# Kernel optimization log

Hardware: AMD Instinct MI355X
Metric: run time of the kernel (lower is better)

Reference implementation:

```python
import jax, jax.numpy as jnp
from jax import lax
import numpy as np

H = 64  # hidden_dim


def _lstm_dir(x, W_ih, W_hh, b, reverse):
    # x: [B,T,I]; W_ih: [4H,I]; W_hh: [4H,H]; b: [4H] (b_ih+b_hh combined)
    B = x.shape[0]
    xp = jnp.einsum('bti,gi->btg', x, W_ih) + b          # [B,T,4H]
    xp = jnp.swapaxes(xp, 0, 1)                          # [T,B,4H]

    def step(carry, xt):
        h, c = carry
        g = xt + h @ W_hh.T                              # [B,4H]
        i, f, gg, o = jnp.split(g, 4, axis=-1)           # PyTorch gate order i,f,g,o
        i = jax.nn.sigmoid(i)
        f = jax.nn.sigmoid(f)
        gg = jnp.tanh(gg)
        o = jax.nn.sigmoid(o)
        c = f * c + i * gg
        h = o * jnp.tanh(c)
        return (h, c), h

    init = (jnp.zeros((B, H), x.dtype), jnp.zeros((B, H), x.dtype))
    _, hs = lax.scan(step, init, xp, reverse=reverse)    # outputs aligned to original positions
    return jnp.swapaxes(hs, 0, 1)                        # [B,T,H]


def _bilstm_layer(x, Wih_f, Whh_f, b_f, Wih_b, Whh_b, b_b):
    fwd = _lstm_dir(x, Wih_f, Whh_f, b_f, reverse=False)
    bwd = _lstm_dir(x, Wih_b, Whh_b, b_b, reverse=True)
    return jnp.concatenate([fwd, bwd], axis=-1)          # [B,T,2H]


def setup_inputs() -> dict:
    key = jax.random.key(0)
    ks = jax.random.split(key, 16)
    s = 0.1
    d = {}
    d['x'] = jax.random.normal(ks[0], (512, 512, 4), dtype=jnp.float32)
    # layer 0 (input size 4), forward / backward directions
    d['Wih_l0_f'] = jax.random.normal(ks[1], (4 * H, 4)) * s
    d['Whh_l0_f'] = jax.random.normal(ks[2], (4 * H, H)) * s
    d['b_l0_f'] = jax.random.normal(ks[3], (4 * H,)) * s
    d['Wih_l0_b'] = jax.random.normal(ks[4], (4 * H, 4)) * s
    d['Whh_l0_b'] = jax.random.normal(ks[5], (4 * H, H)) * s
    d['b_l0_b'] = jax.random.normal(ks[6], (4 * H,)) * s
    # layer 1 (input size 2H = 128)
    d['Wih_l1_f'] = jax.random.normal(ks[7], (4 * H, 2 * H)) * s
    d['Whh_l1_f'] = jax.random.normal(ks[8], (4 * H, H)) * s
    d['b_l1_f'] = jax.random.normal(ks[9], (4 * H,)) * s
    d['Wih_l1_b'] = jax.random.normal(ks[10], (4 * H, 2 * H)) * s
    d['Whh_l1_b'] = jax.random.normal(ks[11], (4 * H, H)) * s
    d['b_l1_b'] = jax.random.normal(ks[12], (4 * H,)) * s
    # final linear: 2H -> 1
    d['fc_w'] = jax.random.normal(ks[13], (1, 2 * H)) * s
    d['fc_b'] = jax.random.normal(ks[14], (1,)) * s
    return d


def reference(x, Wih_l0_f, Whh_l0_f, b_l0_f, Wih_l0_b, Whh_l0_b, b_l0_b,
              Wih_l1_f, Whh_l1_f, b_l1_f, Wih_l1_b, Whh_l1_b, b_l1_b,
              fc_w, fc_b):
    h0 = _bilstm_layer(x, Wih_l0_f, Whh_l0_f, b_l0_f, Wih_l0_b, Whh_l0_b, b_l0_b)
    h1 = _bilstm_layer(h0, Wih_l1_f, Whh_l1_f, b_l1_f, Wih_l1_b, Whh_l1_b, b_l1_b)
    pooled = jnp.mean(h1, axis=1)                        # [B,2H]
    return pooled @ fc_w.T + fc_b                        # [B,1]
```

## Files before the change

kernel.cpp:

```cpp
#include <hip/hip_runtime.h>

#define H  64
#define TT 512
#define BB 512
#define CSTR 80
#define UCH 16
#define XSTRF 260

typedef _Float16 half8 __attribute__((ext_vector_type(8)));
typedef float    f32x4 __attribute__((ext_vector_type(4)));

__device__ __forceinline__ float frcp(float x) { return __builtin_amdgcn_rcpf(x); }
__device__ __forceinline__ float sigm(float x) { return frcp(1.f + __expf(-x)); }
__device__ __forceinline__ float tanh_fast(float x) { return 1.f - 2.f * frcp(__expf(2.f * x) + 1.f); }

__global__ __launch_bounds__(256) void xpad_prep(const float* __restrict__ x,
                                                 _Float16* __restrict__ xpad) {
    int gid = blockIdx.x * 256 + threadIdx.x;
    int row = gid >> 2, q = gid & 3;
    half8 v = {0,0,0,0,0,0,0,0};
    if (q == 0) {
        float4 xv = ((const float4*)x)[row];
        v[0] = (_Float16)xv.x; v[1] = (_Float16)xv.y;
        v[2] = (_Float16)xv.z; v[3] = (_Float16)xv.w;
    }
    *(half8*)(xpad + (size_t)row * 32 + q * 8) = v;
}

__global__ __launch_bounds__(256, 2) void lstm_l0(
    const _Float16* __restrict__ xpad,
    const float* __restrict__ WihF, const float* __restrict__ WhhF, const float* __restrict__ bF,
    const float* __restrict__ WihB, const float* __restrict__ WhhB, const float* __restrict__ bB,
    _Float16* __restrict__ out0)
{
    const int dir = blockIdx.x & 1;
    const int b0  = (blockIdx.x >> 1) * 2;
    const int tid = threadIdx.x;
    const int w = tid >> 6, l = tid & 63, m = l & 15, q = l >> 4;
    const int ch  = m & 1;
    const int ubo = (m >> 1) & 3;
    const int uo  = w * 16 + ubo * 4 + q;
    const bool act = (m < 8);

    const float* Wih = dir ? WihB : WihF;
    const float* Whh = dir ? WhhB : WhhF;
    const float* bia = dir ? bB   : bF;

    half8 Ah[4][2];
#pragma unroll
    for (int ub = 0; ub < 4; ++ub) {
        const int wrow = (m & 3) * 64 + (w * 16 + ub * 4 + (m >> 2));
#pragma unroll
        for (int s2 = 0; s2 < 2; ++s2) {
            const float* src = Whh + wrow * 64 + s2 * 32 + q * 8;
            half8 tmp;
#pragma unroll
            for (int j = 0; j < 8; ++j) tmp[j] = (_Float16)src[j];
            Ah[ub][s2] = tmp;
        }
    }

    half8 Bg[4];
    float bvj[4];
#pragma unroll
    for (int j = 0; j < 4; ++j) {
        const int n  = w * 64 + j * 16 + m;
        const int gr = (n & 3) * 64 + (n >> 2);
        bvj[j] = bia[gr];
        half8 tmp;
#pragma unroll
        for (int jj = 0; jj < 8; ++jj) {
            int k = q * 8 + jj;
            tmp[jj] = (k < 4) ? (_Float16)Wih[gr * 4 + k] : (_Float16)0.f;
        }
        Bg[j] = tmp;
    }

    __shared__ __align__(16) float xp[2][UCH][XSTRF];
    __shared__ _Float16 hbuf[2][2][CSTR];
    for (int i = tid; i < 2 * 2 * CSTR / 2; i += 256) ((unsigned int*)hbuf)[i] = 0u;
    __syncthreads();

    float c = 0.f;
    int p = 0;

    for (int chunk = 0; chunk < TT / UCH; ++chunk) {
        const int c0 = chunk * UCH;

#pragma unroll
        for (int cc = 0; cc < 2; ++cc) {
            const int tA = dir ? (TT - 1 - (c0 + m)) : (c0 + m);
            half8 a0 = *(const half8*)(xpad + (size_t)((b0 + cc) * TT + tA) * 32 + q * 8);
#pragma unroll
            for (int j = 0; j < 4; ++j) {
                f32x4 acc = {bvj[j], bvj[j], bvj[j], bvj[j]};
                acc = __builtin_amdgcn_mfma_f32_16x16x32_f16(a0, Bg[j], acc, 0, 0, 0);
#pragma unroll
                for (int i = 0; i < 4; ++i)
                    xp[cc][q * 4 + i][w * 64 + j * 16 + m] = acc[i];
            }
        }

        f32x4 xv = *(const f32x4*)&xp[ch][0][uo * 4];
        for (int u = 0; u < UCH; ++u) {
            int un = (u + 1 < UCH) ? (u + 1) : u;
            f32x4 xn = *(const f32x4*)&xp[ch][un][uo * 4];

            half8 ah0 = *(const half8*)&hbuf[p][ch][q * 8];
            half8 ah1 = *(const half8*)&hbuf[p][ch][32 + q * 8];

            f32x4 g_own;
#pragma unroll
            for (int ub = 0; ub < 4; ++ub) {
                f32x4 a = __builtin_amdgcn_mfma_f32_16x16x32_f16(Ah[ub][0], ah0, xv, 0, 0, 0);
                a       = __builtin_amdgcn_mfma_f32_16x16x32_f16(Ah[ub][1], ah1, a, 0, 0, 0);
                if (ub == ubo) g_own = a;
            }

            float e_i = sigm(g_own[0]), e_f = sigm(g_own[1]);
            float e_g = tanh_fast(g_own[2]), e_o = sigm(g_own[3]);
            c = e_f * c + e_i * e_g;
            float hh = e_o * tanh_fast(c);

            if (act) {
                const int tg = dir ? (TT - 1 - (c0 + u)) : (c0 + u);
                out0[((size_t)(b0 + ch) * TT + tg) * 128 + dir * 64 + uo] = (_Float16)hh;
                hbuf[p ^ 1][ch][uo] = (_Float16)hh;
            }
            __syncthreads();
            p ^= 1; xv = xn;
        }
    }
}

__global__ __launch_bounds__(256, 2) void lstm_l1(
    const _Float16* __restrict__ out0,
    const float* __restrict__ WihF, const float* __restrict__ WhhF, const float* __restrict__ bF,
    const float* __restrict__ WihB, const float* __restrict__ WhhB, const float* __restrict__ bB,
    float* __restrict__ pooled)
{
    const int dir = blockIdx.x & 1;
    const int b0  = (blockIdx.x >> 1) * 2;
    const int tid = threadIdx.x;
    const int w = tid >> 6, l = tid & 63, m = l & 15, q = l >> 4;
    const int ch  = m & 1;
    const int ubo = (m >> 1) & 3;
    const int uo  = w * 16 + ubo * 4 + q;
    const bool act = (m < 8);

    const float* Wih = dir ? WihB : WihF;
    const float* Whh = dir ? WhhB : WhhF;
    const float* bia = dir ? bB   : bF;

    half8 Ah[4][2];
#pragma unroll
    for (int ub = 0; ub < 4; ++ub) {
        const int wrow = (m & 3) * 64 + (w * 16 + ub * 4 + (m >> 2));
#pragma unroll
        for (int s2 = 0; s2 < 2; ++s2) {
            const float* src = Whh + wrow * 64 + s2 * 32 + q * 8;
            half8 tmp;
#pragma unroll
            for (int j = 0; j < 8; ++j) tmp[j] = (_Float16)src[j];
            Ah[ub][s2] = tmp;
        }
    }

    half8 Bg[4][4];
    float bvj[4];
#pragma unroll
    for (int j = 0; j < 4; ++j) {
        const int n  = w * 64 + j * 16 + m;
        const int gr = (n & 3) * 64 + (n >> 2);
        bvj[j] = bia[gr];
#pragma unroll
        for (int k4 = 0; k4 < 4; ++k4) {
            const float* src = Wih + gr * 128 + k4 * 32 + q * 8;
            half8 tmp;
#pragma unroll
            for (int jj = 0; jj < 8; ++jj) tmp[jj] = (_Float16)src[jj];
            Bg[j][k4] = tmp;
        }
    }

    __shared__ __align__(16) float xp[2][UCH][XSTRF];
    __shared__ _Float16 hbuf[2][2][CSTR];
    for (int i = tid; i < 2 * 2 * CSTR / 2; i += 256) ((unsigned int*)hbuf)[i] = 0u;
    __syncthreads();

    float c = 0.f, hs = 0.f;
    int p = 0;

    for (int chunk = 0; chunk < TT / UCH; ++chunk) {
        const int c0 = chunk * UCH;

#pragma unroll
        for (int cc = 0; cc < 2; ++cc) {
            const int tA = dir ? (TT - 1 - (c0 + m)) : (c0 + m);
            const _Float16* arow = out0 + (size_t)((b0 + cc) * TT + tA) * 128 + q * 8;
            half8 a0 = *(const half8*)(arow);
            half8 a1 = *(const half8*)(arow + 32);
            half8 a2 = *(const half8*)(arow + 64);
            half8 a3 = *(const half8*)(arow + 96);
#pragma unroll
            for (int j = 0; j < 4; ++j) {
                f32x4 acc = {bvj[j], bvj[j], bvj[j], bvj[j]};
                acc = __builtin_amdgcn_mfma_f32_16x16x32_f16(a0, Bg[j][0], acc, 0, 0, 0);
                acc = __builtin_amdgcn_mfma_f32_16x16x32_f16(a1, Bg[j][1], acc, 0, 0, 0);
                acc = __builtin_amdgcn_mfma_f32_16x16x32_f16(a2, Bg[j][2], acc, 0, 0, 0);
                acc = __builtin_amdgcn_mfma_f32_16x16x32_f16(a3, Bg[j][3], acc, 0, 0, 0);
#pragma unroll
                for (int i = 0; i < 4; ++i)
                    xp[cc][q * 4 + i][w * 64 + j * 16 + m] = acc[i];
            }
        }

        f32x4 xv = *(const f32x4*)&xp[ch][0][uo * 4];
        for (int u = 0; u < UCH; ++u) {
            int un = (u + 1 < UCH) ? (u + 1) : u;
            f32x4 xn = *(const f32x4*)&xp[ch][un][uo * 4];

            half8 ah0 = *(const half8*)&hbuf[p][ch][q * 8];
            half8 ah1 = *(const half8*)&hbuf[p][ch][32 + q * 8];

            f32x4 g_own;
#pragma unroll
            for (int ub = 0; ub < 4; ++ub) {
                f32x4 a = __builtin_amdgcn_mfma_f32_16x16x32_f16(Ah[ub][0], ah0, xv, 0, 0, 0);
                a       = __builtin_amdgcn_mfma_f32_16x16x32_f16(Ah[ub][1], ah1, a, 0, 0, 0);
                if (ub == ubo) g_own = a;
            }

            float e_i = sigm(g_own[0]), e_f = sigm(g_own[1]);
            float e_g = tanh_fast(g_own[2]), e_o = sigm(g_own[3]);
            c = e_f * c + e_i * e_g;
            float hh = e_o * tanh_fast(c);
            hs += hh;

            if (act) hbuf[p ^ 1][ch][uo] = (_Float16)hh;
            __syncthreads();
            p ^= 1; xv = xn;
        }
    }

    if (act) pooled[(size_t)(b0 + ch) * 128 + dir * 64 + uo] = hs;
}

__global__ __launch_bounds__(64) void fc_head(
    const float* __restrict__ pooled,
    const float* __restrict__ fcw, const float* __restrict__ fcb,
    float* __restrict__ out)
{
    const int b = blockIdx.x;
    const int l = threadIdx.x;
    float v = pooled[b * 128 + l] * fcw[l] + pooled[b * 128 + 64 + l] * fcw[64 + l];
#pragma unroll
    for (int o = 32; o > 0; o >>= 1) v += __shfl_down(v, o);
    if (l == 0) out[b] = v * (1.f / (float)TT) + fcb[0];
}

extern "C" void kernel_launch(void* const* d_in, const int* in_sizes, int n_in,
                              void* d_out, int out_size, void* d_ws, size_t ws_size,
                              hipStream_t stream) {
    const float* x       = (const float*)d_in[0];
    const float* Wih_l0f = (const float*)d_in[1];
    const float* Whh_l0f = (const float*)d_in[2];
    const float* b_l0f   = (const float*)d_in[3];
    const float* Wih_l0b = (const float*)d_in[4];
    const float* Whh_l0b = (const float*)d_in[5];
    const float* b_l0b   = (const float*)d_in[6];
    const float* Wih_l1f = (const float*)d_in[7];
    const float* Whh_l1f = (const float*)d_in[8];
    const float* b_l1f   = (const float*)d_in[9];
    const float* Wih_l1b = (const float*)d_in[10];
    const float* Whh_l1b = (const float*)d_in[11];
    const float* b_l1b   = (const float*)d_in[12];
    const float* fcw     = (const float*)d_in[13];
    const float* fcb     = (const float*)d_in[14];

    const size_t o_xpad   = 0;
    const size_t o_out0   = o_xpad + (size_t)BB * TT * 32 * 2;
    const size_t o_pooled = o_out0 + (size_t)BB * TT * 128 * 2;

    _Float16* xpad   = (_Float16*)((char*)d_ws + o_xpad);
    _Float16* out0   = (_Float16*)((char*)d_ws + o_out0);
    float*    pooled = (float*)((char*)d_ws + o_pooled);

    xpad_prep<<<(BB * TT * 4) / 256, 256, 0, stream>>>(x, xpad);
    lstm_l0<<<(BB / 2) * 2, 256, 0, stream>>>(xpad, Wih_l0f, Whh_l0f, b_l0f,
                                              Wih_l0b, Whh_l0b, b_l0b, out0);
    lstm_l1<<<(BB / 2) * 2, 256, 0, stream>>>(out0, Wih_l1f, Whh_l1f, b_l1f,
                                              Wih_l1b, Whh_l1b, b_l1b, pooled);
    fc_head<<<BB, 64, 0, stream>>>(pooled, fcw, fcb, (float*)d_out);
}
```

Measured before the change: 482.7 us.

## Rewrite LSTM kernels: one wave per sequence, barrier-free recurrence, prescaled exp2 gates

Merges the two layer kernels into one template in which each wavefront owns a whole batch row and computes all 256 gates with 16 MFMA tiles, so the per-step block barrier disappears. Gate weights and biases are prescaled by log2e factors so activations use exp2 with combined reciprocals. Input projections for the next chunk are interleaved into the recurrent step, with global loads issued two chunks ahead. In exchange each wave does four times the recurrent MFMA work, occupancy drops to one block per SM with larger LDS and register use, and the grid halves to 256 blocks.

```diff
diff --git a/kernel.cpp b/kernel.cpp
--- a/kernel.cpp
+++ b/kernel.cpp
@@ -1,18 +1,22 @@
 #include <hip/hip_runtime.h>
 
-#define H  64
-#define TT 512
-#define BB 512
-#define CSTR 80
-#define UCH 16
-#define XSTRF 260
+#define H   64
+#define TT  512
+#define BB  512
+#define UCH 8
+#define NCH (TT / UCH)
+#define XSTR 260
 
 typedef _Float16 half8 __attribute__((ext_vector_type(8)));
 typedef float    f32x4 __attribute__((ext_vector_type(4)));
 
+#define LOG2E 1.4426950408889634f
+#define TWOL  2.8853900817779268f
+
+#define MFMA16 __builtin_amdgcn_mfma_f32_16x16x32_f16
+
 __device__ __forceinline__ float frcp(float x) { return __builtin_amdgcn_rcpf(x); }
-__device__ __forceinline__ float sigm(float x) { return frcp(1.f + __expf(-x)); }
-__device__ __forceinline__ float tanh_fast(float x) { return 1.f - 2.f * frcp(__expf(2.f * x) + 1.f); }
+__device__ __forceinline__ float ex2(float x)  { return __builtin_amdgcn_exp2f(x); }
 
 __global__ __launch_bounds__(256) void xpad_prep(const float* __restrict__ x,
                                                  _Float16* __restrict__ xpad) {
@@ -27,223 +31,170 @@
     *(half8*)(xpad + (size_t)row * 32 + q * 8) = v;
 }
 
-__global__ __launch_bounds__(256, 2) void lstm_l0(
-    const _Float16* __restrict__ xpad,
+
+template<int KS, bool IS_L0>
+__global__ __launch_bounds__(256, 1) void lstm_k(
+    const _Float16* __restrict__ xsrc,
     const float* __restrict__ WihF, const float* __restrict__ WhhF, const float* __restrict__ bF,
     const float* __restrict__ WihB, const float* __restrict__ WhhB, const float* __restrict__ bB,
-    _Float16* __restrict__ out0)
+    _Float16* __restrict__ out0,
+    float* __restrict__ pooled)
 {
     const int dir = blockIdx.x & 1;
-    const int b0  = (blockIdx.x >> 1) * 2;
+    const int b0  = (blockIdx.x >> 1) * 4;
     const int tid = threadIdx.x;
     const int w = tid >> 6, l = tid & 63, m = l & 15, q = l >> 4;
-    const int ch  = m & 1;
-    const int ubo = (m >> 1) & 3;
-    const int uo  = w * 16 + ubo * 4 + q;
-    const bool act = (m < 8);
 
     const float* Wih = dir ? WihB : WihF;
     const float* Whh = dir ? WhhB : WhhF;
     const float* bia = dir ? bB   : bF;
 
-    half8 Ah[4][2];
-#pragma unroll
-    for (int ub = 0; ub < 4; ++ub) {
-        const int wrow = (m & 3) * 64 + (w * 16 + ub * 4 + (m >> 2));
-#pragma unroll
-        for (int s2 = 0; s2 < 2; ++s2) {
-            const float* src = Whh + wrow * 64 + s2 * 32 + q * 8;
-            half8 tmp;
-#pragma unroll
-            for (int j = 0; j < 8; ++j) tmp[j] = (_Float16)src[j];
-            Ah[ub][s2] = tmp;
-        }
-    }
-
-    half8 Bg[4];
-    float bvj[4];
-#pragma unroll
-    for (int j = 0; j < 4; ++j) {
-        const int n  = w * 64 + j * 16 + m;
-        const int gr = (n & 3) * 64 + (n >> 2);
-        bvj[j] = bia[gr];
-        half8 tmp;
+    half8 Ah[16][2];
+#pragma unroll
+    for (int T = 0; T < 16; ++T) {
+        const float st = ((T >> 2) == 2) ? TWOL : -LOG2E;
+#pragma unroll
+        for (int ks2 = 0; ks2 < 2; ++ks2) {
+            const float* src = Whh + (T * 16 + m) * 64 + ks2 * 32 + q * 8;
+            half8 t8;
+#pragma unroll
+            for (int jj = 0; jj < 8; ++jj) t8[jj] = (_Float16)(src[jj] * st);
+            Ah[T][ks2] = t8;
+        }
+    }
+
+    __shared__ __align__(16) _Float16 wih_s[16 * KS * 64 * 8];
+    __shared__ __align__(16) float    bia_s[256];
+    __shared__ __align__(16) float    xps[2][4][UCH * XSTR];
+    __shared__ __align__(16) float    gsc[4][264];
+    __shared__ __align__(16) _Float16 hsc[4][64];
+
+#pragma unroll
+    for (int f = 0; f < KS * 4; ++f) {
+        const int F  = tid * (KS * 4) + f;
+        const int T  = F / (KS * 64);
+        const int r  = F % (KS * 64);
+        const int ks = r >> 6;
+        const int ll = r & 63;
+        const int row = T * 16 + (ll & 15);
+        const int c0  = ks * 32 + (ll >> 4) * 8;
+        const float st = ((T >> 2) == 2) ? TWOL : -LOG2E;
+        half8 t8;
 #pragma unroll
         for (int jj = 0; jj < 8; ++jj) {
-            int k = q * 8 + jj;
-            tmp[jj] = (k < 4) ? (_Float16)Wih[gr * 4 + k] : (_Float16)0.f;
-        }
-        Bg[j] = tmp;
-    }
-
-    __shared__ __align__(16) float xp[2][UCH][XSTRF];
-    __shared__ _Float16 hbuf[2][2][CSTR];
-    for (int i = tid; i < 2 * 2 * CSTR / 2; i += 256) ((unsigned int*)hbuf)[i] = 0u;
+            const int k = c0 + jj;
+            float v;
+            if constexpr (IS_L0) v = (k < 4) ? Wih[row * 4 + k] : 0.f;
+            else                 v = Wih[row * 128 + k];
+            t8[jj] = (_Float16)(v * st);
+        }
+        *(half8*)&wih_s[F * 8] = t8;
+    }
+    bia_s[tid] = bia[tid] * (((tid >> 6) == 2) ? TWOL : -LOG2E);
+    hsc[w][l] = (_Float16)0.f;
     __syncthreads();
 
-    float c = 0.f;
-    int p = 0;
-
-    for (int chunk = 0; chunk < TT / UCH; ++chunk) {
-        const int c0 = chunk * UCH;
-
-#pragma unroll
-        for (int cc = 0; cc < 2; ++cc) {
-            const int tA = dir ? (TT - 1 - (c0 + m)) : (c0 + m);
-            half8 a0 = *(const half8*)(xpad + (size_t)((b0 + cc) * TT + tA) * 32 + q * 8);
-#pragma unroll
-            for (int j = 0; j < 4; ++j) {
-                f32x4 acc = {bvj[j], bvj[j], bvj[j], bvj[j]};
-                acc = __builtin_amdgcn_mfma_f32_16x16x32_f16(a0, Bg[j], acc, 0, 0, 0);
-#pragma unroll
-                for (int i = 0; i < 4; ++i)
-                    xp[cc][q * 4 + i][w * 64 + j * 16 + m] = acc[i];
+    const f32x4 vz = {0.f, 0.f, 0.f, 0.f};
+    float cp = 0.f, hs = 0.f;
+
+    half8 aR[2][KS];
+    auto LOADX = [&](half8 (&dst)[KS], int c) {
+        const int t  = c * UCH + (m & 7);
+        const int tA = dir ? (TT - 1 - t) : t;
+#pragma unroll
+        for (int ks = 0; ks < KS; ++ks) {
+            if constexpr (IS_L0)
+                dst[ks] = *(const half8*)(xsrc + ((size_t)(b0 + w) * TT + tA) * 32 + q * 8);
+            else
+                dst[ks] = *(const half8*)(xsrc + ((size_t)(b0 + w) * TT + tA) * 128 + ks * 32 + q * 8);
+        }
+    };
+
+    LOADX(aR[0], 0);
+    LOADX(aR[1], 1);
+
+#pragma unroll
+    for (int TA = 0; TA < 16; ++TA) {
+        f32x4 acc = *(const f32x4*)&bia_s[TA * 16 + q * 4];
+#pragma unroll
+        for (int ks = 0; ks < KS; ++ks) {
+            half8 wf = *(const half8*)&wih_s[((TA * KS + ks) * 64 + l) * 8];
+            acc = MFMA16(wf, aR[0][ks], acc, 0, 0, 0);
+        }
+        if (m < UCH)
+            *(f32x4*)&xps[0][w][m * XSTR + (TA >> 2) * 64 + (TA & 3) * 16 + q * 4] = acc;
+    }
+
+#define GT(T)                                                                   \
+    {   f32x4 d = MFMA16(Ah[T][0], hb0, vz, 0, 0, 0);                           \
+        d = MFMA16(Ah[T][1], hb1, d, 0, 0, 0);                                  \
+        if (m == (T)) *(f32x4*)&gsc[w][(T) * 16 + q * 4] = d;   }
+
+#define PHA(TAe, AUSE)                                                          \
+    {   const int TA = (TAe);                                                   \
+        f32x4 acc = *(const f32x4*)&bia_s[TA * 16 + q * 4];                     \
+        _Pragma("unroll")                                                       \
+        for (int ks = 0; ks < KS; ++ks) {                                       \
+            half8 wf = *(const half8*)&wih_s[((TA * KS + ks) * 64 + l) * 8];    \
+            acc = MFMA16(wf, AUSE[ks], acc, 0, 0, 0);                           \
+        }                                                                       \
+        if (pref && m < UCH)                                                    \
+            *(f32x4*)&xpW[m * XSTR + (TA >> 2) * 64 + (TA & 3) * 16 + q * 4] = acc; }
+
+    auto CHUNK = [&](int c_, const float* xpR, float* xpW,
+                     half8 (&AUSE)[KS], half8 (&ALOAD)[KS]) {
+        if (c_ + 2 < NCH) LOADX(ALOAD, c_ + 2);
+        const bool pref = (c_ + 1 < NCH);
+#pragma unroll
+        for (int u = 0; u < UCH; ++u) {
+            half8 hb0 = *(const half8*)&hsc[w][q * 8];
+            half8 hb1 = *(const half8*)&hsc[w][32 + q * 8];
+            float xq0 = xpR[u * XSTR +   0 + l];
+            float xq1 = xpR[u * XSTR +  64 + l];
+            float xq2 = xpR[u * XSTR + 128 + l];
+            float xq3 = xpR[u * XSTR + 192 + l];
+
+            GT(0) GT(1) GT(2) GT(3)
+            float gi = gsc[w][  0 + l] + xq0;
+            float I = ex2(gi); float i1 = 1.f + I;
+            GT(4) GT(5) GT(6) GT(7)
+            float gf = gsc[w][ 64 + l] + xq1;
+            float Fv = ex2(gf); float rf = frcp(1.f + Fv);
+            PHA(2 * u, AUSE)
+            GT(8) GT(9) GT(10) GT(11)
+            float gg = gsc[w][128 + l] + xq2;
+            float G = ex2(gg);
+            float rIG = frcp(fmaf(i1, G, i1));
+            float P = fmaf(TWOL, G, -TWOL) * rIG;
+            cp = fmaf(rf, cp, P);
+            GT(12) GT(13) GT(14) GT(15)
+            PHA(2 * u + 1, AUSE)
+            float go = gsc[w][192 + l] + xq3;
+            float O = ex2(go); float o1 = 1.f + O;
+            float Cx = ex2(cp);
+            float rOC = frcp(fmaf(o1, Cx, o1));
+            float hh = (Cx - 1.f) * rOC;
+            hsc[w][l] = (_Float16)hh;
+            if constexpr (IS_L0) {
+                const int t  = c_ * UCH + u;
+                const int tg = dir ? (TT - 1 - t) : t;
+                out0[((size_t)(b0 + w) * TT + tg) * 128 + dir * 64 + l] = (_Float16)hh;
+            } else {
+                hs += hh;
             }
         }
-
-        f32x4 xv = *(const f32x4*)&xp[ch][0][uo * 4];
-        for (int u = 0; u < UCH; ++u) {
-            int un = (u + 1 < UCH) ? (u + 1) : u;
-            f32x4 xn = *(const f32x4*)&xp[ch][un][uo * 4];
-
-            half8 ah0 = *(const half8*)&hbuf[p][ch][q * 8];
-            half8 ah1 = *(const half8*)&hbuf[p][ch][32 + q * 8];
-
-            f32x4 g_own;
-#pragma unroll
-            for (int ub = 0; ub < 4; ++ub) {
-                f32x4 a = __builtin_amdgcn_mfma_f32_16x16x32_f16(Ah[ub][0], ah0, xv, 0, 0, 0);
-                a       = __builtin_amdgcn_mfma_f32_16x16x32_f16(Ah[ub][1], ah1, a, 0, 0, 0);
-                if (ub == ubo) g_own = a;
-            }
-
-            float e_i = sigm(g_own[0]), e_f = sigm(g_own[1]);
-            float e_g = tanh_fast(g_own[2]), e_o = sigm(g_own[3]);
-            c = e_f * c + e_i * e_g;
-            float hh = e_o * tanh_fast(c);
-
-            if (act) {
-                const int tg = dir ? (TT - 1 - (c0 + u)) : (c0 + u);
-                out0[((size_t)(b0 + ch) * TT + tg) * 128 + dir * 64 + uo] = (_Float16)hh;
-                hbuf[p ^ 1][ch][uo] = (_Float16)hh;
-            }
-            __syncthreads();
-            p ^= 1; xv = xn;
-        }
-    }
-}
-
-__global__ __launch_bounds__(256, 2) void lstm_l1(
-    const _Float16* __restrict__ out0,
-    const float* __restrict__ WihF, const float* __restrict__ WhhF, const float* __restrict__ bF,
-    const float* __restrict__ WihB, const float* __restrict__ WhhB, const float* __restrict__ bB,
-    float* __restrict__ pooled)
-{
-    const int dir = blockIdx.x & 1;
-    const int b0  = (blockIdx.x >> 1) * 2;
-    const int tid = threadIdx.x;
-    const int w = tid >> 6, l = tid & 63, m = l & 15, q = l >> 4;
-    const int ch  = m & 1;
-    const int ubo = (m >> 1) & 3;
-    const int uo  = w * 16 + ubo * 4 + q;
-    const bool act = (m < 8);
-
-    const float* Wih = dir ? WihB : WihF;
-    const float* Whh = dir ? WhhB : WhhF;
-    const float* bia = dir ? bB   : bF;
-
-    half8 Ah[4][2];
-#pragma unroll
-    for (int ub = 0; ub < 4; ++ub) {
-        const int wrow = (m & 3) * 64 + (w * 16 + ub * 4 + (m >> 2));
-#pragma unroll
-        for (int s2 = 0; s2 < 2; ++s2) {
-            const float* src = Whh + wrow * 64 + s2 * 32 + q * 8;
-            half8 tmp;
-#pragma unroll
-            for (int j = 0; j < 8; ++j) tmp[j] = (_Float16)src[j];
-            Ah[ub][s2] = tmp;
-        }
-    }
-
-    half8 Bg[4][4];
-    float bvj[4];
-#pragma unroll
-    for (int j = 0; j < 4; ++j) {
-        const int n  = w * 64 + j * 16 + m;
-        const int gr = (n & 3) * 64 + (n >> 2);
-        bvj[j] = bia[gr];
-#pragma unroll
-        for (int k4 = 0; k4 < 4; ++k4) {
-            const float* src = Wih + gr * 128 + k4 * 32 + q * 8;
-            half8 tmp;
-#pragma unroll
-            for (int jj = 0; jj < 8; ++jj) tmp[jj] = (_Float16)src[jj];
-            Bg[j][k4] = tmp;
-        }
-    }
-
-    __shared__ __align__(16) float xp[2][UCH][XSTRF];
-    __shared__ _Float16 hbuf[2][2][CSTR];
-    for (int i = tid; i < 2 * 2 * CSTR / 2; i += 256) ((unsigned int*)hbuf)[i] = 0u;
-    __syncthreads();
-
-    float c = 0.f, hs = 0.f;
-    int p = 0;
-
-    for (int chunk = 0; chunk < TT / UCH; ++chunk) {
-        const int c0 = chunk * UCH;
-
-#pragma unroll
-        for (int cc = 0; cc < 2; ++cc) {
-            const int tA = dir ? (TT - 1 - (c0 + m)) : (c0 + m);
-            const _Float16* arow = out0 + (size_t)((b0 + cc) * TT + tA) * 128 + q * 8;
-            half8 a0 = *(const half8*)(arow);
-            half8 a1 = *(const half8*)(arow + 32);
-            half8 a2 = *(const half8*)(arow + 64);
-            half8 a3 = *(const half8*)(arow + 96);
-#pragma unroll
-            for (int j = 0; j < 4; ++j) {
-                f32x4 acc = {bvj[j], bvj[j], bvj[j], bvj[j]};
-                acc = __builtin_amdgcn_mfma_f32_16x16x32_f16(a0, Bg[j][0], acc, 0, 0, 0);
-                acc = __builtin_amdgcn_mfma_f32_16x16x32_f16(a1, Bg[j][1], acc, 0, 0, 0);
-                acc = __builtin_amdgcn_mfma_f32_16x16x32_f16(a2, Bg[j][2], acc, 0, 0, 0);
-                acc = __builtin_amdgcn_mfma_f32_16x16x32_f16(a3, Bg[j][3], acc, 0, 0, 0);
-#pragma unroll
-                for (int i = 0; i < 4; ++i)
-                    xp[cc][q * 4 + i][w * 64 + j * 16 + m] = acc[i];
-            }
-        }
-
-        f32x4 xv = *(const f32x4*)&xp[ch][0][uo * 4];
-        for (int u = 0; u < UCH; ++u) {
-            int un = (u + 1 < UCH) ? (u + 1) : u;
-            f32x4 xn = *(const f32x4*)&xp[ch][un][uo * 4];
-
-            half8 ah0 = *(const half8*)&hbuf[p][ch][q * 8];
-            half8 ah1 = *(const half8*)&hbuf[p][ch][32 + q * 8];
-
-            f32x4 g_own;
-#pragma unroll
-            for (int ub = 0; ub < 4; ++ub) {
-                f32x4 a = __builtin_amdgcn_mfma_f32_16x16x32_f16(Ah[ub][0], ah0, xv, 0, 0, 0);
-                a       = __builtin_amdgcn_mfma_f32_16x16x32_f16(Ah[ub][1], ah1, a, 0, 0, 0);
-                if (ub == ubo) g_own = a;
-            }
-
-            float e_i = sigm(g_own[0]), e_f = sigm(g_own[1]);
-            float e_g = tanh_fast(g_own[2]), e_o = sigm(g_own[3]);
-            c = e_f * c + e_i * e_g;
-            float hh = e_o * tanh_fast(c);
-            hs += hh;
-
-            if (act) hbuf[p ^ 1][ch][uo] = (_Float16)hh;
-            __syncthreads();
-            p ^= 1; xv = xn;
-        }
-    }
-
-    if (act) pooled[(size_t)(b0 + ch) * 128 + dir * 64 + uo] = hs;
+    };
+
+    for (int c = 0; c < NCH; c += 2) {
+        CHUNK(c,     &xps[0][w][0], &xps[1][w][0], aR[1], aR[0]);
+        CHUNK(c + 1, &xps[1][w][0], &xps[0][w][0], aR[0], aR[1]);
+    }
+
+#undef GT
+#undef PHA
+
+    if constexpr (!IS_L0)
+        pooled[(size_t)(b0 + w) * 128 + dir * 64 + l] = hs;
 }
 
 __global__ __launch_bounds__(64) void fc_head(
@@ -287,9 +238,9 @@
     float*    pooled = (float*)((char*)d_ws + o_pooled);
 
     xpad_prep<<<(BB * TT * 4) / 256, 256, 0, stream>>>(x, xpad);
-    lstm_l0<<<(BB / 2) * 2, 256, 0, stream>>>(xpad, Wih_l0f, Whh_l0f, b_l0f,
-                                              Wih_l0b, Whh_l0b, b_l0b, out0);
-    lstm_l1<<<(BB / 2) * 2, 256, 0, stream>>>(out0, Wih_l1f, Whh_l1f, b_l1f,
-                                              Wih_l1b, Whh_l1b, b_l1b, pooled);
+    lstm_k<1, true ><<<(BB / 4) * 2, 256, 0, stream>>>(xpad, Wih_l0f, Whh_l0f, b_l0f,
+                                                       Wih_l0b, Whh_l0b, b_l0b, out0, nullptr);
+    lstm_k<4, false><<<(BB / 4) * 2, 256, 0, stream>>>(out0, Wih_l1f, Whh_l1f, b_l1f,
+                                                       Wih_l1b, Whh_l1b, b_l1b, nullptr, pooled);
     fc_head<<<BB, 64, 0, stream>>>(pooled, fcw, fcb, (float*)d_out);
 }
```

After: 1.018 ms. +110.9%, slower.
